# Performance work log

Measured on AMD Instinct MI355X. Metric: run time of the kernel, lower is better.

Reference implementation:

```python
import jax, jax.numpy as jnp
import numpy as np

NEG_SLOPE = 0.2
MASK_FILL = -1e9


def setup_inputs() -> dict:
    key = jax.random.key(0)
    k1, k2, k3, k4 = jax.random.split(key, 4)
    B, N, IN_DIM = 4, 2048, 256
    H, D = 8, 64  # n_heads, hidden_dim (out_dim)
    nodes = jax.random.normal(k1, (B, N, IN_DIM), dtype=jnp.float32)
    edges = jax.random.randint(k2, (B, N, N), 0, 2, dtype=jnp.int32)
    # Xavier-uniform-ish init for params
    pw_lim = float(np.sqrt(6.0 / (IN_DIM + H * D)))
    proj_weights = jax.random.uniform(k3, (IN_DIM, H * D), dtype=jnp.float32,
                                      minval=-pw_lim, maxval=pw_lim)
    aw_lim = float(np.sqrt(6.0 / (H + 2 * D)))
    attn_weights = jax.random.uniform(k4, (H, 2 * D), dtype=jnp.float32,
                                      minval=-aw_lim, maxval=aw_lim)
    return {"nodes": nodes, "edges": edges,
            "proj_weights": proj_weights, "attn_weights": attn_weights}


def reference(nodes, edges, proj_weights, attn_weights):
    B, N, _ = nodes.shape
    H, twoD = attn_weights.shape
    D = twoD // 2
    # Projection: [B,N,in] @ [in,H*D] -> [B,H,N,D]
    mapped = jnp.matmul(nodes, proj_weights).reshape(B, N, H, D).transpose(0, 2, 1, 3)
    # The left@diag(a)@right^T trick is exactly a_l.h_i + a_r.h_j:
    a_l = attn_weights[:, :D]   # [H,D]
    a_r = attn_weights[:, D:]   # [H,D]
    el = jnp.einsum('bhnd,hd->bhn', mapped, a_l)  # score contribution of source i
    er = jnp.einsum('bhnd,hd->bhn', mapped, a_r)  # score contribution of target j
    scores = jax.nn.leaky_relu(el[:, :, :, None] + er[:, :, None, :],
                               negative_slope=NEG_SLOPE)  # [B,H,N,N]
    scores = jnp.where(edges[:, None, :, :] == 0, MASK_FILL, scores)
    attn = jax.nn.softmax(scores, axis=-1)  # dropout p=0 -> identity
    out = jnp.einsum('bhij,bhjd->bhid', attn, mapped)  # [B,H,N,D]
    out = out.transpose(0, 2, 1, 3).reshape(B, N, H * D)  # is_concat=True
    return jax.nn.sigmoid(out)
```

## Files before the change

kernel.cpp:

```cpp
#include <hip/hip_runtime.h>
#include <hip/hip_fp16.h>
#include <math.h>

#define NEG 0.2f
#define LOG2E 1.4426950408889634f

typedef float f32x4 __attribute__((ext_vector_type(4)));
typedef _Float16 half8 __attribute__((ext_vector_type(8)));
typedef _Float16 h2v __attribute__((ext_vector_type(2)));
typedef short s16x2 __attribute__((ext_vector_type(2)));

#if __has_builtin(__builtin_amdgcn_exp2f)
#define EXP2F(x) __builtin_amdgcn_exp2f(x)
#else
#define EXP2F(x) exp2f(x)
#endif

__device__ inline uint cvt2(float a, float b) {
  union {
    decltype(__builtin_amdgcn_cvt_pkrtz(0.f, 0.f)) v;
    uint u;
  } x;
  x.v = __builtin_amdgcn_cvt_pkrtz(a, b);
  return x.u;
}

__device__ inline h2v u2h(uint u) {
  union {
    uint u;
    h2v v;
  } x;
  x.u = u;
  return x.v;
}

__device__ inline uint h2u(h2v v) {
  union {
    uint u;
    h2v v;
  } x;
  x.v = v;
  return x.u;
}

__device__ inline uint sgn16(uint t) {
  union {
    uint u;
    s16x2 v;
  } x;
  x.u = t;
  x.v = x.v >> 15;
  return x.u;
}


__device__ inline void pack4_mlp(const int* __restrict__ e, uint* __restrict__ epk32,
                                 size_t g0, int l) {
  int4 v0 = *(const int4*)(e + (g0 + 0) * 256 + l * 4);
  int4 v1 = *(const int4*)(e + (g0 + 1) * 256 + l * 4);
  int4 v2 = *(const int4*)(e + (g0 + 2) * 256 + l * 4);
  int4 v3 = *(const int4*)(e + (g0 + 3) * 256 + l * 4);
#define PK1(k, vv)                                 \
  {                                                \
    unsigned long long b0 = __ballot(vv.x != 0);   \
    unsigned long long b1 = __ballot(vv.y != 0);   \
    unsigned long long b2 = __ballot(vv.z != 0);   \
    unsigned long long b3 = __ballot(vv.w != 0);   \
    if (l == 0) {                                  \
      uint4 lo, hi;                                \
      lo.x = (uint)b0;                             \
      lo.y = (uint)b1;                             \
      lo.z = (uint)b2;                             \
      lo.w = (uint)b3;                             \
      hi.x = (uint)(b0 >> 32);                     \
      hi.y = (uint)(b1 >> 32);                     \
      hi.z = (uint)(b2 >> 32);                     \
      hi.w = (uint)(b3 >> 32);                     \
      *(uint4*)&epk32[(g0 + k) * 8] = lo;          \
      *(uint4*)&epk32[(g0 + k) * 8 + 4] = hi;      \
    }                                              \
  }
  PK1(0, v0)
  PK1(1, v1)
  PK1(2, v2)
  PK1(3, v3)
#undef PK1
}

__global__ __launch_bounds__(256, 4) void prep_pack(
    const float* __restrict__ W, ushort* __restrict__ wf, uint* __restrict__ ermx,
    const int* __restrict__ e, uint* __restrict__ epk32) {
  const int bx = blockIdx.x;
  const int t = threadIdx.x;
  const int l = t & 63;
  if (bx < 33) {
    if (bx == 32) {
      if (t < 32) ermx[t] = 0u;
      return;
    }
    const int h = bx >> 2, ct = bx & 3;
#pragma unroll
    for (int s = 0; s < 2; ++s) {
      int slot = t + s * 256;
      int ll = slot & 63, kk = slot >> 6;
      int col = h * 64 + ct * 16 + (ll & 15);
      int k0 = kk * 32 + (ll >> 4) * 8;
      uint outv[4];
#pragma unroll
      for (int c = 0; c < 4; ++c) {
        float x0 = W[(size_t)(k0 + 2 * c) * 512 + col];
        float x1 = W[(size_t)(k0 + 2 * c + 1) * 512 + col];
        outv[c] = cvt2(x0, x1);
      }
      *(uint4*)&wf[(((size_t)((h * 4 + ct) * 8 + kk)) * 64 + ll) * 8] = *(uint4*)outv;
    }
    return;
  }
  const size_t g0 = (size_t)(bx - 33) * 16 + (t >> 6) * 4;
  pack4_mlp(e, epk32, g0, l);
}

__global__ __launch_bounds__(256, 4) void pack2_proj(
    const int* __restrict__ e, uint* __restrict__ epk32,
    const float* __restrict__ A, const ushort* __restrict__ wf,
    const float* __restrict__ aw, ushort* __restrict__ mt,
    float* __restrict__ el, float* __restrict__ er, uint* __restrict__ ermx) {
  __shared__ ushort ct_lds[64][72];
  const int bx = blockIdx.x;
  const int t = threadIdx.x;
  const int l = t & 63;
  if (bx % 3 != 2) {
    const int pb = (bx / 3) * 2 + (bx % 3);
    const size_t g0 = 32768 + (size_t)pb * 16 + (t >> 6) * 4;
    pack4_mlp(e, epk32, g0, l);
    return;
  }
  const int pid = bx / 3;
  const int wq = t >> 6;
  const int i0 = (pid & 127) * 64;
  const int h = pid >> 7;
  const int b = i0 >> 11, n0 = i0 & 2047, bh = b * 8 + h;
  const int cl = l & 15, hi = l >> 4;
  const float* arow = A + (size_t)(i0 + wq * 16 + cl) * 256 + hi * 8;
  const int4* wfb = (const int4*)wf + (size_t)h * 32 * 64 + l;
  f32x4 acc[4];
#pragma unroll
  for (int ct = 0; ct < 4; ++ct) acc[ct] = (f32x4){0.f, 0.f, 0.f, 0.f};
#pragma unroll
  for (int kk = 0; kk < 8; ++kk) {
    float4 a0 = *(const float4*)(arow + kk * 32);
    float4 a1 = *(const float4*)(arow + kk * 32 + 4);
    union {
      uint u[4];
      half8 v;
    } af;
    af.u[0] = cvt2(a0.x, a0.y);
    af.u[1] = cvt2(a0.z, a0.w);
    af.u[2] = cvt2(a1.x, a1.y);
    af.u[3] = cvt2(a1.z, a1.w);
#pragma unroll
    for (int ct = 0; ct < 4; ++ct) {
      union {
        int4 i;
        half8 v;
      } bf;
      bf.i = wfb[((size_t)ct * 8 + kk) * 64];
      acc[ct] = __builtin_amdgcn_mfma_f32_16x16x32_f16(af.v, bf.v, acc[ct], 0, 0, 0);
    }
  }
  float alc[4], arc[4];
#pragma unroll
  for (int ct = 0; ct < 4; ++ct) {
    alc[ct] = aw[h * 128 + ct * 16 + cl];
    arc[ct] = aw[h * 128 + 64 + ct * 16 + cl];
  }
  float ermax_loc = -1e30f;
#pragma unroll
  for (int reg = 0; reg < 4; ++reg) {
    float pl = acc[0][reg] * alc[0] + acc[1][reg] * alc[1] + acc[2][reg] * alc[2] +
               acc[3][reg] * alc[3];
    float pr = acc[0][reg] * arc[0] + acc[1][reg] * arc[1] + acc[2][reg] * arc[2] +
               acc[3][reg] * arc[3];
#pragma unroll
    for (int s = 1; s < 16; s <<= 1) {
      pl += __shfl_xor(pl, s);
      pr += __shfl_xor(pr, s);
    }
    if (cl == 0) {
      int n = n0 + wq * 16 + hi * 4 + reg;
      el[(size_t)bh * 2048 + n] = pl;
      er[(size_t)bh * 2048 + n] = pr;
    }
    ermax_loc = fmaxf(ermax_loc, pr);
  }
  ermax_loc = fmaxf(ermax_loc, __shfl_xor(ermax_loc, 16));
  ermax_loc = fmaxf(ermax_loc, __shfl_xor(ermax_loc, 32));
  if (l == 0) {
    uint bits = __float_as_uint(ermax_loc);
    uint key = (bits & 0x80000000u) ? ~bits : (bits | 0x80000000u);
    atomicMax(&ermx[bh], key);
  }
#pragma unroll
  for (int ct = 0; ct < 4; ++ct) {
    ushort4 us;
    us.x = __half_as_ushort(__float2half(acc[ct][0]));
    us.y = __half_as_ushort(__float2half(acc[ct][1]));
    us.z = __half_as_ushort(__float2half(acc[ct][2]));
    us.w = __half_as_ushort(__float2half(acc[ct][3]));
    *(ushort4*)&ct_lds[ct * 16 + cl][wq * 16 + hi * 4] = us;
  }
  __syncthreads();
  {
    const int f = t >> 5, s = t & 31;
    const int g = f >> 2, nt = f & 3;
    const int r = nt * 16 + (s & 15);
    const int cm = g * 32 + (s >> 4) * 8;
    int4 v0 = *(const int4*)&ct_lds[r][cm];
    int4 v1 = *(const int4*)&ct_lds[r][cm + 16];
    const size_t base = ((size_t)bh * 32 + (n0 >> 6)) * 4096 + f * 512;
    *(int4*)&mt[base + s * 8] = v0;
    *(int4*)&mt[base + (s + 32) * 8] = v1;
  }
}

__global__ __launch_bounds__(256, 4) void gat_attn(
    const ushort* __restrict__ mt, const uint* __restrict__ epk32,
    const float* __restrict__ el, const float* __restrict__ er,
    const uint* __restrict__ ermx, float* __restrict__ out) {
  __shared__ __align__(16) char smem[24576];
  int4* vt4 = (int4*)smem;
  uint* ysh = (uint*)(smem + 16384);
  uint* vsh = (uint*)(smem + 20480);
  const int t = threadIdx.x;
  const int l = t & 63;
  const int wq = t >> 6;
  const int r16 = l & 15, hi = l >> 4;
  const int bid = blockIdx.x;
  const int nb = (bid & 7) * 128 + (bid >> 3);
  const int i0 = (nb & 31) * 64;
  const int h = (nb >> 5) & 7;
  const int b = nb >> 8;
  const int bh = b * 8 + h;
  const uint ky = ermx[bh];
  const float emx = __uint_as_float((ky & 0x80000000u) ? (ky ^ 0x80000000u) : ~ky);
  {
    float4 e0 = *(const float4*)&er[(size_t)bh * 2048 + t * 8];
    float4 e1 = *(const float4*)&er[(size_t)bh * 2048 + t * 8 + 4];
    uint4 yp, vp;
    yp.x = cvt2(EXP2F((e0.x - emx) * LOG2E), EXP2F((e0.y - emx) * LOG2E));
    yp.y = cvt2(EXP2F((e0.z - emx) * LOG2E), EXP2F((e0.w - emx) * LOG2E));
    yp.z = cvt2(EXP2F((e1.x - emx) * LOG2E), EXP2F((e1.y - emx) * LOG2E));
    yp.w = cvt2(EXP2F((e1.z - emx) * LOG2E), EXP2F((e1.w - emx) * LOG2E));
    vp.x = cvt2(EXP2F((e0.x - emx) * (NEG * LOG2E)), EXP2F((e0.y - emx) * (NEG * LOG2E)));
    vp.y = cvt2(EXP2F((e0.z - emx) * (NEG * LOG2E)), EXP2F((e0.w - emx) * (NEG * LOG2E)));
    vp.z = cvt2(EXP2F((e1.x - emx) * (NEG * LOG2E)), EXP2F((e1.y - emx) * (NEG * LOG2E)));
    vp.w = cvt2(EXP2F((e1.z - emx) * (NEG * LOG2E)), EXP2F((e1.w - emx) * (NEG * LOG2E)));
    *(uint4*)&ysh[t * 4] = yp;
    *(uint4*)&vsh[t * 4] = vp;
  }
  const int irow = i0 + wq * 16 + r16;
  h2v X2, U2;
  {
    const float s0 = el[(size_t)bh * 2048 + irow] + emx;
    const float m2 = fmaxf(s0, NEG * s0) * LOG2E;
    const float Xf = EXP2F(s0 * LOG2E - m2);
    const float Uf = EXP2F(NEG * s0 * LOG2E - m2);
    X2 = u2h(cvt2(Xf, Xf));
    U2 = u2h(cvt2(Uf, Uf));
  }
  const uint* prow = epk32 + (size_t)(b * 2048 + irow) * 64;
  f32x4 acc[4];
  f32x4 accL = {0.f, 0.f, 0.f, 0.f};
#pragma unroll
  for (int nt = 0; nt < 4; ++nt) acc[nt] = (f32x4){0.f, 0.f, 0.f, 0.f};
  half8 ones;
#pragma unroll
  for (int c = 0; c < 8; ++c) ones[c] = (_Float16)1.f;

  const int4* srcbase = (const int4*)mt + (size_t)bh * 32 * 512 + wq * 128 + l;
  uint4 epw = *(const uint4*)&prow[0];
  {
    int4 p0 = srcbase[0];
    int4 p1 = srcbase[64];
    int4* d = vt4 + wq * 128 + l;
    d[0] = p0;
    d[64] = p1;
  }
  __syncthreads();
  int cur = 0;
  for (int jt = 0; jt < 32; ++jt) {
    int4 nx0, nx1;
    uint4 epwn;
    if (jt < 31) {
      const int4* s = srcbase + (size_t)(jt + 1) * 512;
      nx0 = s[0];
      nx1 = s[64];
      const int jn = jt + 1;
      epwn = *(const uint4*)&prow[((jn >> 2) << 3) + (((jn >> 1) & 1) << 2)];
    }
    half8 af[2];
#pragma unroll
    for (int g = 0; g < 2; ++g) {
      const uint idx = jt * 32 + g * 16 + hi * 4;
      uint4 y4 = *(const uint4*)&ysh[idx];
      uint4 v4 = *(const uint4*)&vsh[idx];
      const uint bsh = ((jt & 1) << 4) + (g << 3) + hi * 2;
      const uint p0 = epw.x >> bsh, p1 = epw.y >> bsh;
      const uint p2 = epw.z >> bsh, p3 = epw.w >> bsh;
      union {
        uint u[4];
        half8 v8;
      } fr;
      fr.u[0] = h2u(__builtin_elementwise_max(X2 * u2h(y4.x), U2 * u2h(v4.x))) &
                sgn16(((p0 & 1u) << 15) | (p1 << 31));
      fr.u[1] = h2u(__builtin_elementwise_max(X2 * u2h(y4.y), U2 * u2h(v4.y))) &
                sgn16(((p2 & 1u) << 15) | (p3 << 31));
      fr.u[2] = h2u(__builtin_elementwise_max(X2 * u2h(y4.z), U2 * u2h(v4.z))) &
                sgn16((((p0 >> 1) & 1u) << 15) | ((p1 >> 1) << 31));
      fr.u[3] = h2u(__builtin_elementwise_max(X2 * u2h(y4.w), U2 * u2h(v4.w))) &
                sgn16((((p2 >> 1) & 1u) << 15) | ((p3 >> 1) << 31));
      af[g] = fr.v8;
    }
    const half8* fb = (const half8*)(vt4 + cur * 512);
    __builtin_amdgcn_s_setprio(1);
#pragma unroll
    for (int g = 0; g < 2; ++g) {
      accL = __builtin_amdgcn_mfma_f32_16x16x32_f16(af[g], ones, accL, 0, 0, 0);
#pragma unroll
      for (int nt = 0; nt < 4; ++nt) {
        half8 bfr = fb[(g * 4 + nt) * 64 + l];
        acc[nt] = __builtin_amdgcn_mfma_f32_16x16x32_f16(af[g], bfr, acc[nt], 0, 0, 0);
      }
    }
    __builtin_amdgcn_s_setprio(0);
    if (jt < 31) {
      int4* d = vt4 + (cur ^ 1) * 512 + wq * 128 + l;
      d[0] = nx0;
      d[64] = nx1;
      epw = epwn;
    }
    __syncthreads();
    cur ^= 1;
  }
#pragma unroll
  for (int reg = 0; reg < 4; ++reg) {
    float invL = 1.f / accL[reg];
    int orow = i0 + wq * 16 + hi * 4 + reg;
#pragma unroll
    for (int nt = 0; nt < 4; ++nt) {
      float o = acc[nt][reg] * invL;
      float sig = 1.f / (1.f + __expf(-o));
      out[(size_t)(b * 2048 + orow) * 512 + h * 64 + nt * 16 + r16] = sig;
    }
  }
}

extern "C" void kernel_launch(void* const* d_in, const int* in_sizes, int n_in,
                              void* d_out, int out_size, void* d_ws, size_t ws_size,
                              hipStream_t stream) {
  const float* nodes = (const float*)d_in[0];
  const int* edges = (const int*)d_in[1];
  const float* pw = (const float*)d_in[2];
  const float* aw = (const float*)d_in[3];
  float* out = (float*)d_out;

  ushort* mt = (ushort*)d_ws;
  float* el = (float*)((char*)d_ws + 8388608);
  float* er = (float*)((char*)d_ws + 8650752);
  uint* ermx = (uint*)((char*)d_ws + 8912896);
  uint* epk = (uint*)((char*)d_ws + 8913024);
  ushort* wf = (ushort*)((char*)d_ws + 11010176);

  prep_pack<<<2081, 256, 0, stream>>>(pw, wf, ermx, edges, epk);
  pack2_proj<<<3072, 256, 0, stream>>>(edges, epk, nodes, wf, aw, mt, el, er, ermx);
  gat_attn<<<1024, 256, 0, stream>>>(mt, epk, el, er, ermx, out);
}
```

Baseline: 86.97 us.

## Double attention block rows to 128 with 512 threads sharing V tiles

The attention kernel now launches 512 threads (8 waves) per block covering 128 query rows instead of 64, with half as many blocks. Each thread loads one int4 of the shared V tile per step instead of two, and each block computes the exponentiated er tables once for twice as many rows. This halves the global-to-LDS V traffic and the per-block setup cost. In exchange, larger barriers synchronize more waves per step and the launch bound of 8 may limit registers.

Result: no change. 87.83 us (+1.0%).

```diff
diff --git a/kernel.cpp b/kernel.cpp
--- a/kernel.cpp
+++ b/kernel.cpp
@@ -223,7 +223,7 @@
   }
 }
 
-__global__ __launch_bounds__(256, 4) void gat_attn(
+__global__ __launch_bounds__(512, 8) void gat_attn(
     const ushort* __restrict__ mt, const uint* __restrict__ epk32,
     const float* __restrict__ el, const float* __restrict__ er,
     const uint* __restrict__ ermx, float* __restrict__ out) {
@@ -236,27 +236,22 @@
   const int wq = t >> 6;
   const int r16 = l & 15, hi = l >> 4;
   const int bid = blockIdx.x;
-  const int nb = (bid & 7) * 128 + (bid >> 3);
-  const int i0 = (nb & 31) * 64;
-  const int h = (nb >> 5) & 7;
-  const int b = nb >> 8;
+  const int nb = (bid & 7) * 64 + (bid >> 3);
+  const int i0 = (nb & 15) * 128;
+  const int h = (nb >> 4) & 7;
+  const int b = nb >> 7;
   const int bh = b * 8 + h;
   const uint ky = ermx[bh];
   const float emx = __uint_as_float((ky & 0x80000000u) ? (ky ^ 0x80000000u) : ~ky);
   {
-    float4 e0 = *(const float4*)&er[(size_t)bh * 2048 + t * 8];
-    float4 e1 = *(const float4*)&er[(size_t)bh * 2048 + t * 8 + 4];
-    uint4 yp, vp;
+    float4 e0 = *(const float4*)&er[(size_t)bh * 2048 + t * 4];
+    uint2 yp, vp;
     yp.x = cvt2(EXP2F((e0.x - emx) * LOG2E), EXP2F((e0.y - emx) * LOG2E));
     yp.y = cvt2(EXP2F((e0.z - emx) * LOG2E), EXP2F((e0.w - emx) * LOG2E));
-    yp.z = cvt2(EXP2F((e1.x - emx) * LOG2E), EXP2F((e1.y - emx) * LOG2E));
-    yp.w = cvt2(EXP2F((e1.z - emx) * LOG2E), EXP2F((e1.w - emx) * LOG2E));
     vp.x = cvt2(EXP2F((e0.x - emx) * (NEG * LOG2E)), EXP2F((e0.y - emx) * (NEG * LOG2E)));
     vp.y = cvt2(EXP2F((e0.z - emx) * (NEG * LOG2E)), EXP2F((e0.w - emx) * (NEG * LOG2E)));
-    vp.z = cvt2(EXP2F((e1.x - emx) * (NEG * LOG2E)), EXP2F((e1.y - emx) * (NEG * LOG2E)));
-    vp.w = cvt2(EXP2F((e1.z - emx) * (NEG * LOG2E)), EXP2F((e1.w - emx) * (NEG * LOG2E)));
-    *(uint4*)&ysh[t * 4] = yp;
-    *(uint4*)&vsh[t * 4] = vp;
+    *(uint2*)&ysh[t * 2] = yp;
+    *(uint2*)&vsh[t * 2] = vp;
   }
   const int irow = i0 + wq * 16 + r16;
   h2v X2, U2;
@@ -277,24 +272,18 @@
 #pragma unroll
   for (int c = 0; c < 8; ++c) ones[c] = (_Float16)1.f;
 
-  const int4* srcbase = (const int4*)mt + (size_t)bh * 32 * 512 + wq * 128 + l;
+  const int4* srcbase = (const int4*)mt + (size_t)bh * 32 * 512 + t;
   uint4 epw = *(const uint4*)&prow[0];
   {
-    int4 p0 = srcbase[0];
-    int4 p1 = srcbase[64];
-    int4* d = vt4 + wq * 128 + l;
-    d[0] = p0;
-    d[64] = p1;
+    vt4[t] = srcbase[0];
   }
   __syncthreads();
   int cur = 0;
   for (int jt = 0; jt < 32; ++jt) {
-    int4 nx0, nx1;
+    int4 nx0;
     uint4 epwn;
     if (jt < 31) {
-      const int4* s = srcbase + (size_t)(jt + 1) * 512;
-      nx0 = s[0];
-      nx1 = s[64];
+      nx0 = srcbase[(size_t)(jt + 1) * 512];
       const int jn = jt + 1;
       epwn = *(const uint4*)&prow[((jn >> 2) << 3) + (((jn >> 1) & 1) << 2)];
     }
@@ -334,9 +323,8 @@
     }
     __builtin_amdgcn_s_setprio(0);
     if (jt < 31) {
-      int4* d = vt4 + (cur ^ 1) * 512 + wq * 128 + l;
-      d[0] = nx0;
-      d[64] = nx1;
+      int4* d = vt4 + (cur ^ 1) * 512;
+      d[t] = nx0;
       epw = epwn;
     }
     __syncthreads();
@@ -373,5 +361,5 @@
 
   prep_pack<<<2081, 256, 0, stream>>>(pw, wf, ermx, edges, epk);
   pack2_proj<<<3072, 256, 0, stream>>>(edges, epk, nodes, wf, aw, mt, el, er, ermx);
-  gat_attn<<<1024, 256, 0, stream>>>(mt, epk, el, er, ermx, out);
-}
+  gat_attn<<<512, 512, 0, stream>>>(mt, epk, el, er, ermx, out);
+}
```
